# Kernel optimization log

Measured on AMD Instinct MI355X. Metric: run time of the kernel, lower is better.

## Reference

```python
import jax, jax.numpy as jnp
import numpy as np

D_MODEL = 1024
D_STATE = 16
D_CONV = 4
EXPAND = 2
D_INNER = EXPAND * D_MODEL          # 2048
DT_RANK = D_MODEL // 16             # 64 (math.ceil(d_model/16))
BATCH, SEQLEN = 2, 1024


def setup_inputs() -> dict:
    key = jax.random.key(0)
    ks = jax.random.split(key, 9)
    f32 = jnp.float32
    hidden_states = jax.random.normal(ks[0], (BATCH, SEQLEN, D_MODEL), dtype=f32)
    in_proj_w = jax.random.normal(ks[1], (2 * D_INNER, D_MODEL), dtype=f32) * (D_MODEL ** -0.5)
    conv1d_w = jax.random.normal(ks[2], (D_INNER, D_CONV), dtype=f32) * (D_CONV ** -0.5)
    conv1d_b = jax.random.normal(ks[3], (D_INNER,), dtype=f32) * 0.1
    x_proj_w = jax.random.normal(ks[4], (DT_RANK + 2 * D_STATE, D_INNER), dtype=f32) * (D_INNER ** -0.5)
    dt_std = DT_RANK ** -0.5
    dt_proj_w = jax.random.uniform(ks[5], (D_INNER, DT_RANK), dtype=f32, minval=-dt_std, maxval=dt_std)
    dt_proj_b = jax.random.normal(ks[6], (D_INNER,), dtype=f32) * 0.1
    # A = repeat(arange(1, d_state+1), 'n -> d n'); A_log = log(A)
    A_log = jnp.log(jnp.tile(jnp.arange(1, D_STATE + 1, dtype=f32), (D_INNER, 1)))
    D_param = jnp.ones((D_INNER,), dtype=f32)
    out_proj_w = jax.random.normal(ks[7], (D_MODEL, D_INNER), dtype=f32) * (D_INNER ** -0.5)
    return dict(hidden_states=hidden_states, in_proj_w=in_proj_w, conv1d_w=conv1d_w,
                conv1d_b=conv1d_b, x_proj_w=x_proj_w, dt_proj_w=dt_proj_w,
                dt_proj_b=dt_proj_b, A_log=A_log, D_param=D_param, out_proj_w=out_proj_w)


def _mamba_fwd(hidden_states, in_proj_w, conv1d_w, conv1d_b, x_proj_w,
               dt_proj_w, dt_proj_b, A_log, D_param, out_proj_w):
    Bsz, L, _ = hidden_states.shape
    # in_proj: (B,L,d_model) -> (B,L,2*d_inner); split into x, z
    xz = jnp.einsum('bld,ed->ble', hidden_states, in_proj_w)
    x, z = jnp.split(xz, 2, axis=-1)                      # each (B,L,d_inner)
    # causal depthwise conv1d over L (left pad d_conv-1), then SiLU (fused in causal_conv1d_fwd)
    xc = jnp.transpose(x, (0, 2, 1))                      # (B,d_inner,L)
    kern = conv1d_w[:, None, :]                           # (d_inner,1,d_conv)
    conv = jax.lax.conv_general_dilated(
        xc, kern, window_strides=(1,), padding=[(D_CONV - 1, 0)],
        dimension_numbers=('NCH', 'OIH', 'NCH'), feature_group_count=D_INNER)
    u = jax.nn.silu(conv + conv1d_b[None, :, None])       # (B,d_inner,L)
    ut = jnp.transpose(u, (0, 2, 1))                      # (B,L,d_inner)
    # x_proj -> [dt | B | C]
    x_dbl = jnp.einsum('bld,rd->blr', ut, x_proj_w)       # (B,L,dt_rank+2*d_state)
    dt_low = x_dbl[..., :DT_RANK]
    B_var = x_dbl[..., DT_RANK:DT_RANK + D_STATE]         # (B,L,d_state)
    C_var = x_dbl[..., DT_RANK + D_STATE:]                # (B,L,d_state)
    # delta = softplus(dt_proj_w @ dt_low + dt_proj_b)  (delta_bias applied inside selective scan)
    delta = jax.nn.softplus(jnp.einsum('blr,dr->bld', dt_low, dt_proj_w) + dt_proj_b)  # (B,L,d_inner)
    A = -jnp.exp(A_log)                                   # (d_inner,d_state)
    # discretize: h_l = exp(delta*A) * h_{l-1} + (delta*B_l) * u_l
    dA = jnp.exp(delta[..., None] * A)                    # (B,L,d_inner,d_state)
    dBu = delta[..., None] * B_var[:, :, None, :] * ut[..., None]  # (B,L,d_inner,d_state)

    def step(h, inp):
        da, dbu, c = inp
        h = da * h + dbu                                  # (B,d_inner,d_state)
        y = jnp.einsum('bdn,bn->bd', h, c)
        return h, y

    h0 = jnp.zeros((Bsz, D_INNER, D_STATE), dtype=hidden_states.dtype)
    _, ys = jax.lax.scan(step, h0, (jnp.moveaxis(dA, 1, 0),
                                    jnp.moveaxis(dBu, 1, 0),
                                    jnp.moveaxis(C_var, 1, 0)))
    y = jnp.moveaxis(ys, 0, 1)                            # (B,L,d_inner)
    y = y + ut * D_param                                  # skip term D*u
    out_z = y * jax.nn.silu(z)                            # gated output
    return jnp.einsum('bld,ed->ble', out_z, out_proj_w)   # (B,L,d_model)


def reference(hidden_states, in_proj_w, conv1d_w, conv1d_b, x_proj_w,
              dt_proj_w, dt_proj_b, A_log, D_param, out_proj_w):
    return _mamba_fwd(hidden_states, in_proj_w, conv1d_w, conv1d_b, x_proj_w,
                      dt_proj_w, dt_proj_b, A_log, D_param, out_proj_w)
```

## Files before the change

kernel.cpp:

```cpp
#include <hip/hip_runtime.h>
#include <hip/hip_bf16.h>

#define BATCH 2
#define SEQLEN 1024
#define DMODEL 1024
#define DINNER 2048
#define DSTATE 16
#define DTRANK 64
#define ROWS (BATCH * SEQLEN)
#define LOG2E 1.44269504088896340736f

using bf16 = __hip_bfloat16;
typedef __bf16 bf16x8 __attribute__((ext_vector_type(8)));
typedef float f32x4 __attribute__((ext_vector_type(4)));
typedef unsigned short us8 __attribute__((ext_vector_type(8)));

__device__ __forceinline__ float to_f(float x) { return x; }
__device__ __forceinline__ float to_f(bf16 x) { return __bfloat162float(x); }

__device__ __forceinline__ float fexp2(float x) { return __builtin_amdgcn_exp2f(x); }

__device__ __forceinline__ float bfu(unsigned short u) {
    union { unsigned int i; float f; } v;
    v.i = ((unsigned int)u) << 16;
    return v.f;
}

__device__ __forceinline__ unsigned short bf_bits(float x) {
    bf16 h = __float2bfloat16(x);
    union { bf16 b; unsigned short u; } cv;
    cv.b = h;
    return cv.u;
}

__device__ __forceinline__ float softplus_f(float x) {
    return fmaxf(x, 0.f) + log1pf(expf(-fabsf(x)));
}
__device__ __forceinline__ float silu_f(float x) {
    return x * __builtin_amdgcn_rcpf(1.f + fexp2(-x * LOG2E));
}

template <int CTRL>
__device__ __forceinline__ float dpp_shr(float x) {
    int r = __builtin_amdgcn_update_dpp(0, __builtin_bit_cast(int, x), CTRL, 0xF, 0xF, false);
    return __builtin_bit_cast(float, r);
}
__device__ __forceinline__ float row16_sum_to_lane15(float p) {
    p += dpp_shr<0x111>(p);
    p += dpp_shr<0x112>(p);
    p += dpp_shr<0x114>(p);
    p += dpp_shr<0x118>(p);
    return p;
}

__device__ __forceinline__ void gload16(const void* g, void* l) {
    __builtin_amdgcn_global_load_lds(
        (const __attribute__((address_space(1))) void*)g,
        (__attribute__((address_space(3))) void*)l, 16, 0, 0);
}

__global__ __launch_bounds__(256) void prep_kernel(const unsigned short* hs, int* flag,
                                                   float* zbuf, int nzero) {
    if (blockIdx.x == 0) {
        __shared__ int cnt[256];
        int c = 0;
        for (int i = threadIdx.x; i < 8192; i += 256) {
            int e = (hs[i] >> 7) & 0xFF;
            if (e == 0 || e == 0xFF || e < 96 || e > 159) c++;
        }
        cnt[threadIdx.x] = c;
        __syncthreads();
        for (int s = 128; s > 0; s >>= 1) {
            if (threadIdx.x < s) cnt[threadIdx.x] += cnt[threadIdx.x + s];
            __syncthreads();
        }
        if (threadIdx.x == 0) *flag = (cnt[0] < 512) ? 1 : 0;
    } else {
        int i = (blockIdx.x - 1) * 256 + threadIdx.x;
        if (i < nzero) zbuf[i] = 0.f;
    }
}

struct SrcPtrs { const void* p[10]; };

__device__ __constant__ const size_t SEG_OFF[11] = {
    0, 2097152, 6291456, 6299648, 6301696, 6498304,
    6629376, 6631424, 6664192, 6666240, 8763392
};

__global__ __launch_bounds__(256) void convert_all(SrcPtrs s, bf16* __restrict__ dst,
                                                   const int* __restrict__ flag) {
    size_t e = ((size_t)blockIdx.x * 256 + threadIdx.x) * 4;
    if (e >= SEG_OFF[10]) return;
    int seg = 0;
    #pragma unroll
    for (int i = 1; i < 10; ++i) if (e >= SEG_OFF[i]) seg = i;
    int isbf = *flag;
    if (isbf && (seg == 0 || seg == 1 || seg == 9)) return;
    size_t loc = e - SEG_OFF[seg];
    if (isbf) {
        ushort4 v = ((const ushort4*)s.p[seg])[loc / 4];
        ((ushort4*)(dst + e))[0] = v;
    } else {
        float4 v = ((const float4*)s.p[seg])[loc / 4];
        ushort4 o;
        o.x = bf_bits(v.x); o.y = bf_bits(v.y);
        o.z = bf_bits(v.z); o.w = bf_bits(v.w);
        ((ushort4*)(dst + e))[0] = o;
    }
}

template <int OUTMODE>
__global__ __launch_bounds__(256) void gemm_mfma(
    const bf16* __restrict__ A, int lda,
    const bf16* __restrict__ Bm, int ldb,
    void* __restrict__ C, int ldc,
    int Kspl, size_t pstride,
    const bf16* __restrict__ bias,
    const bf16* __restrict__ Aalt,
    const bf16* __restrict__ Balt,
    const int* __restrict__ flag)
{
    if (flag && *flag) {
        if (Aalt) A = Aalt;
        if (Balt) Bm = Balt;
    }
    __shared__ __align__(16) __bf16 sA[128 * 32];
    __shared__ __align__(16) __bf16 sB[128 * 32];
    const int tid = threadIdx.x;
    const int m0 = blockIdx.y * 128;
    const int n0 = blockIdx.x * 128;
    const int wid = tid >> 6, ln = tid & 63;
    const int wy = (wid >> 1) * 64, wx = (wid & 1) * 64;
    const int q = ln >> 4, m16 = ln & 15;
    const int kbeg = blockIdx.z * Kspl;

    f32x4 acc[4][4] = {};

    for (int k0 = kbeg; k0 < kbeg + Kspl; k0 += 32) {
        #pragma unroll
        for (int i = 0; i < 2; ++i) {
            int idx = tid + i * 256;
            int r = idx >> 2, c = (idx & 3) * 8;
            gload16(&A[(size_t)(m0 + r) * lda + k0 + c], &sA[idx * 8]);
        }
        #pragma unroll
        for (int i = 0; i < 2; ++i) {
            int idx = tid + i * 256;
            int r = idx >> 2, c = (idx & 3) * 8;
            gload16(&Bm[(size_t)(n0 + r) * ldb + k0 + c], &sB[idx * 8]);
        }
        __syncthreads();
        bf16x8 a[4], b[4];
        #pragma unroll
        for (int i = 0; i < 4; ++i)
            a[i] = *(const bf16x8*)&sA[(wy + i * 16 + m16) * 32 + q * 8];
        #pragma unroll
        for (int j = 0; j < 4; ++j)
            b[j] = *(const bf16x8*)&sB[(wx + j * 16 + m16) * 32 + q * 8];
        #pragma unroll
        for (int i = 0; i < 4; ++i)
            #pragma unroll
            for (int j = 0; j < 4; ++j)
                acc[i][j] = __builtin_amdgcn_mfma_f32_16x16x32_bf16(a[i], b[j], acc[i][j], 0, 0, 0);
        __syncthreads();
    }

    #pragma unroll
    for (int i = 0; i < 4; ++i) {
        #pragma unroll
        for (int j = 0; j < 4; ++j) {
            #pragma unroll
            for (int r = 0; r < 4; ++r) {
                int row = m0 + wy + i * 16 + q * 4 + r;
                int col = n0 + wx + j * 16 + m16;
                size_t idx = (size_t)row * ldc + col;
                float v = acc[i][j][r];
                if constexpr (OUTMODE == 0) {
                    ((bf16*)C)[idx] = __float2bfloat16(v);
                } else if constexpr (OUTMODE == 2) {
                    ((float*)C + blockIdx.z * pstride)[idx] = v;
                } else if constexpr (OUTMODE == 3) {
                    if (col < 96) atomicAdd((float*)C + idx, v);
                } else if constexpr (OUTMODE == 4) {
                    ((float*)C)[idx] = softplus_f(v + to_f(bias[row]));
                }
            }
        }
    }
}

__global__ __launch_bounds__(256) void dt_gemm(
    const bf16* __restrict__ dtw,
    const float* __restrict__ xd,
    const bf16* __restrict__ bias,
    float* __restrict__ deltaT)
{
    const int tid = threadIdx.x;
    const int wid = tid >> 6, ln = tid & 63;
    const int q = ln >> 4, m16 = ln & 15;
    const int n0 = blockIdx.x * 16;
    const int m0 = (blockIdx.y * 4 + wid) * 16;

    const ushort* ap = (const ushort*)dtw + (size_t)(m0 + m16) * 64 + q * 8;
    bf16x8 a0 = *(const bf16x8*)(ap);
    bf16x8 a1 = *(const bf16x8*)(ap + 32);

    const float* bp = xd + (size_t)(n0 + m16) * 96 + q * 8;
    float4 f0 = *(const float4*)(bp);
    float4 f1 = *(const float4*)(bp + 4);
    float4 f2 = *(const float4*)(bp + 32);
    float4 f3 = *(const float4*)(bp + 36);
    union { bf16x8 v; ushort u[8]; } b0c, b1c;
    b0c.u[0] = bf_bits(f0.x); b0c.u[1] = bf_bits(f0.y);
    b0c.u[2] = bf_bits(f0.z); b0c.u[3] = bf_bits(f0.w);
    b0c.u[4] = bf_bits(f1.x); b0c.u[5] = bf_bits(f1.y);
    b0c.u[6] = bf_bits(f1.z); b0c.u[7] = bf_bits(f1.w);
    b1c.u[0] = bf_bits(f2.x); b1c.u[1] = bf_bits(f2.y);
    b1c.u[2] = bf_bits(f2.z); b1c.u[3] = bf_bits(f2.w);
    b1c.u[4] = bf_bits(f3.x); b1c.u[5] = bf_bits(f3.y);
    b1c.u[6] = bf_bits(f3.z); b1c.u[7] = bf_bits(f3.w);

    f32x4 acc = {};
    acc = __builtin_amdgcn_mfma_f32_16x16x32_bf16(a0, b0c.v, acc, 0, 0, 0);
    acc = __builtin_amdgcn_mfma_f32_16x16x32_bf16(a1, b1c.v, acc, 0, 0, 0);

    const int d0 = m0 + q * 4;
    ushort4 bb = *(const ushort4*)((const ushort*)bias + d0);
    float bv[4] = {bfu(bb.x), bfu(bb.y), bfu(bb.z), bfu(bb.w)};
    #pragma unroll
    for (int r = 0; r < 4; ++r) {
        deltaT[(size_t)(d0 + r) * ROWS + n0 + m16] = softplus_f(acc[r] + bv[r]);
    }
}

__global__ __launch_bounds__(256) void sum_store(
    const float* __restrict__ p0, const float* __restrict__ p1,
    void* __restrict__ out, const int* __restrict__ flag, int n4)
{
    int i = blockIdx.x * 256 + threadIdx.x;
    if (i >= n4) return;
    float4 a = ((const float4*)p0)[i];
    float4 b = ((const float4*)p1)[i];
    float4 sv; sv.x = a.x + b.x; sv.y = a.y + b.y; sv.z = a.z + b.z; sv.w = a.w + b.w;
    if (*flag) {
        ushort4 o;
        o.x = bf_bits(sv.x); o.y = bf_bits(sv.y);
        o.z = bf_bits(sv.z); o.w = bf_bits(sv.w);
        ((ushort4*)out)[i] = o;
    } else {
        ((float4*)out)[i] = sv;
    }
}

__global__ __launch_bounds__(256) void transpose_bf16(
    const ushort* __restrict__ src,
    ushort* __restrict__ dst)
{
    __shared__ ushort t[64][65];
    const int bx = blockIdx.x;
    const int by = blockIdx.y;
    const int tid = threadIdx.x;
    const int lr = tid & 63;
    const int ld = tid >> 6;
    #pragma unroll
    for (int i = 0; i < 16; ++i) {
        int d = ld + i * 4;
        t[d][lr] = src[(size_t)(by * 64 + d) * ROWS + bx * 64 + lr];
    }
    __syncthreads();
    #pragma unroll
    for (int i = 0; i < 16; ++i) {
        int r = ld + i * 4;
        dst[(size_t)(bx * 64 + r) * DINNER + by * 64 + lr] = t[lr][r];
    }
}

__global__ __launch_bounds__(256) void conv_silu_fused(
    const bf16* __restrict__ xzT,
    const bf16* __restrict__ w,
    const bf16* __restrict__ bias,
    bf16* __restrict__ utT,
    ushort* __restrict__ ut)
{
    __shared__ ushort sx[64][68];
    __shared__ ushort tt[64][65];
    const int bx = blockIdx.x;
    const int by = blockIdx.y;
    const int tid = threadIdx.x;
    const int gr0 = bx * 64;
    const bool seqstart = (bx & 15) == 0;

    for (int idx = tid; idx < 64 * 17; idx += 256) {
        int row = idx / 17;
        int c = idx - row * 17;
        ushort4 v;
        if (c == 0 && seqstart) {
            v.x = v.y = v.z = v.w = 0;
        } else {
            const ushort* src = (const ushort*)xzT +
                (size_t)(by * 64 + row) * ROWS + (gr0 - 4 + c * 4);
            v = *(const ushort4*)src;
        }
        *(ushort4*)&sx[row][c * 4] = v;
    }
    __syncthreads();

    const int lr = tid & 63;
    const int ld = tid >> 6;
    #pragma unroll
    for (int i = 0; i < 16; ++i) {
        int dl = ld + i * 4;
        int dg = by * 64 + dl;
        ushort4 wv = *(const ushort4*)((const ushort*)w + dg * 4);
        float w0 = bfu(wv.x), w1 = bfu(wv.y), w2 = bfu(wv.z), w3 = bfu(wv.w);
        float bv = to_f(bias[dg]);
        float acc = bv;
        acc = fmaf(bfu(sx[dl][lr + 1]), w0, acc);
        acc = fmaf(bfu(sx[dl][lr + 2]), w1, acc);
        acc = fmaf(bfu(sx[dl][lr + 3]), w2, acc);
        acc = fmaf(bfu(sx[dl][lr + 4]), w3, acc);
        ushort o = bf_bits(silu_f(acc));
        ((ushort*)utT)[(size_t)dg * ROWS + gr0 + lr] = o;
        tt[dl][lr] = o;
    }
    __syncthreads();
    #pragma unroll
    for (int i = 0; i < 16; ++i) {
        int rl = ld + i * 4;
        ut[(size_t)(gr0 + rl) * DINNER + by * 64 + lr] = tt[lr][rl];
    }
}

#define SCHUNK 8
#define SSTEPS (SEQLEN / SCHUNK)
__global__ __launch_bounds__(512) void scan_kernel16(
    const float* __restrict__ deltaT,
    const bf16*  __restrict__ utT,
    const float* __restrict__ xd96,
    const bf16*  __restrict__ xzT,
    const bf16*  __restrict__ A_log,
    const bf16*  __restrict__ Dp,
    bf16* __restrict__ outzT)
{
    __shared__ float2 sHP[SCHUNK][64];
    const int tid = threadIdx.x;
    const int c = tid >> 6;
    const int w = tid & 63;
    const int dcol = (tid >> 4) & 3;
    const int n = tid & 15;
    const int b = blockIdx.x >> 9;
    const int d = ((blockIdx.x & 511) << 2) + dcol;
    const int row0 = b * SEQLEN + c * SSTEPS;

    const float Aa2 = -expf(to_f(A_log[d * DSTATE + n])) * LOG2E;
    const float Dv = to_f(Dp[d]);

    const float*  dp = deltaT + (size_t)d * ROWS + row0;
    const ushort* up = (const ushort*)utT + (size_t)d * ROWS + row0;
    const ushort* zp = (const ushort*)xzT + (size_t)(DINNER + d) * ROWS + row0;
    const float*  bcp = xd96 + (size_t)row0 * 96 + 64 + n;

    float hl = 0.f, sd = 0.f;
    float4  dv4 = *(const float4*)(dp);
    ushort4 uv4 = *(const ushort4*)(up);
    const float* bct = bcp;
    for (int i0 = 0; i0 < SSTEPS; i0 += 4) {
        float4  dvn = *(const float4*)(dp + i0 + 4);
        ushort4 uvn = *(const ushort4*)(up + i0 + 4);
        float Bv[4];
        Bv[0] = bct[0];
        Bv[1] = bct[96];
        Bv[2] = bct[192];
        Bv[3] = bct[288];
        bct += 384;
        float dv[4] = {dv4.x, dv4.y, dv4.z, dv4.w};
        float uv[4] = {bfu(uv4.x), bfu(uv4.y), bfu(uv4.z), bfu(uv4.w)};
        #pragma unroll
        for (int j = 0; j < 4; ++j) {
            sd += dv[j];
            float a = fexp2(dv[j] * Aa2);
            hl = fmaf(a, hl, dv[j] * Bv[j] * uv[j]);
        }
        dv4 = dvn; uv4 = uvn;
    }
    sHP[c][w] = make_float2(hl, fexp2(sd * Aa2));
    __syncthreads();

    float hin = 0.f;
    for (int cc = 0; cc < c; ++cc) {
        float2 hp = sHP[cc][w];
        hin = fmaf(hp.y, hin, hp.x);
    }

    float h = hin;
    dv4 = *(const float4*)(dp);
    uv4 = *(const ushort4*)(up);
    ushort4 zv4 = *(const ushort4*)(zp);
    bct = bcp;
    for (int i0 = 0; i0 < SSTEPS; i0 += 4) {
        float4  dvn = *(const float4*)(dp + i0 + 4);
        ushort4 uvn = *(const ushort4*)(up + i0 + 4);
        ushort4 zvn = *(const ushort4*)(zp + i0 + 4);
        float Bv[4], Cv[4];
        Bv[0] = bct[0];   Cv[0] = bct[16];
        Bv[1] = bct[96];  Cv[1] = bct[112];
        Bv[2] = bct[192]; Cv[2] = bct[208];
        Bv[3] = bct[288]; Cv[3] = bct[304];
        bct += 384;
        float dv[4] = {dv4.x, dv4.y, dv4.z, dv4.w};
        float uv[4] = {bfu(uv4.x), bfu(uv4.y), bfu(uv4.z), bfu(uv4.w)};
        float zv[4] = {bfu(zv4.x), bfu(zv4.y), bfu(zv4.z), bfu(zv4.w)};
        float y[4];
        #pragma unroll
        for (int j = 0; j < 4; ++j) {
            float a = fexp2(dv[j] * Aa2);
            h = fmaf(a, h, dv[j] * Bv[j] * uv[j]);
            float p = h * Cv[j];
            p = row16_sum_to_lane15(p);
            y[j] = fmaf(uv[j], Dv, p);
        }
        if (n == 15) {
            ushort4 o;
            o.x = bf_bits(y[0] * silu_f(zv[0]));
            o.y = bf_bits(y[1] * silu_f(zv[1]));
            o.z = bf_bits(y[2] * silu_f(zv[2]));
            o.w = bf_bits(y[3] * silu_f(zv[3]));
            *(ushort4*)((ushort*)outzT + (size_t)d * ROWS + row0 + i0) = o;
        }
        dv4 = dvn; uv4 = uvn; zv4 = zvn;
    }
}

extern "C" void kernel_launch(void* const* d_in, const int* in_sizes, int n_in,
                              void* d_out, int out_size, void* d_ws, size_t ws_size,
                              hipStream_t stream) {
    static const size_t SZ[10] = {
        (size_t)BATCH * SEQLEN * DMODEL,
        (size_t)2 * DINNER * DMODEL,
        (size_t)DINNER * 4,
        (size_t)DINNER,
        (size_t)(DTRANK + 2 * DSTATE) * DINNER,
        (size_t)DINNER * DTRANK,
        (size_t)DINNER,
        (size_t)DINNER * DSTATE,
        (size_t)DINNER,
        (size_t)DMODEL * DINNER
    };
    size_t tot_in = 0;
    for (int i = 0; i < 10; ++i) tot_in += SZ[i];

    char* p = (char*)d_ws;
    int* flag = (int*)p;                     p += 64;
    bf16* inb = (bf16*)p;                    p += tot_in * 2;
    bf16* xzT = (bf16*)p;                    p += (size_t)4096 * ROWS * 2;
    bf16* utT = (bf16*)p;                    p += (size_t)DINNER * ROWS * 2;
    bf16* ut  = (bf16*)p;                    p += (size_t)ROWS * DINNER * 2;
    float* xd = (float*)p;                   p += (size_t)ROWS * 96 * 4;
    float* deltaT = (float*)p;               p += (size_t)DINNER * ROWS * 4;
    bf16* outzT = (bf16*)p;                  p += (size_t)DINNER * ROWS * 2;
    bf16* outz = (bf16*)p;                   p += (size_t)ROWS * DINNER * 2;
    float* part = (float*)p;                 p += (size_t)2 * ROWS * DMODEL * 4;
    size_t needed = (size_t)(p - (char*)d_ws);
    if (ws_size < needed) return;

    dim3 blk(256);

    prep_kernel<<<1 + (ROWS * 96 + 255) / 256, blk, 0, stream>>>(
        (const unsigned short*)d_in[0], flag, xd, ROWS * 96);

    bf16* inp[10];
    {
        size_t off = 0;
        for (int i = 0; i < 10; ++i) { inp[i] = inb + off; off += SZ[i]; }
    }
    SrcPtrs sp;
    for (int i = 0; i < 10; ++i) sp.p[i] = d_in[i];
    convert_all<<<(int)((tot_in / 4 + 255) / 256), blk, 0, stream>>>(sp, inb, flag);

    const bf16* hs        = inp[0];
    const bf16* in_proj_w = inp[1];
    const bf16* conv_w    = inp[2];
    const bf16* conv_b    = inp[3];
    const bf16* x_proj_w  = inp[4];
    const bf16* dt_proj_w = inp[5];
    const bf16* dt_proj_b = inp[6];
    const bf16* A_log     = inp[7];
    const bf16* Dp        = inp[8];
    const bf16* out_proj_w= inp[9];

    gemm_mfma<0><<<dim3(ROWS / 128, 4096 / 128, 1), blk, 0, stream>>>(
        in_proj_w, DMODEL, hs, DMODEL, xzT, ROWS, DMODEL, 0, nullptr,
        (const bf16*)d_in[1], (const bf16*)d_in[0], flag);

    conv_silu_fused<<<dim3(ROWS / 64, DINNER / 64), blk, 0, stream>>>(
        xzT, conv_w, conv_b, utT, (ushort*)ut);

    gemm_mfma<3><<<dim3(1, ROWS / 128, 16), blk, 0, stream>>>(
        ut, DINNER, x_proj_w, DINNER, xd, 96, DINNER / 16, 0, nullptr,
        nullptr, nullptr, nullptr);

    dt_gemm<<<dim3(ROWS / 16, DINNER / 64), blk, 0, stream>>>(
        dt_proj_w, xd, dt_proj_b, deltaT);

    scan_kernel16<<<BATCH * (DINNER / 4), dim3(512), 0, stream>>>(
        deltaT, utT, xd, xzT, A_log, Dp, outzT);

    transpose_bf16<<<dim3(ROWS / 64, DINNER / 64), blk, 0, stream>>>(
        (const ushort*)outzT, (ushort*)outz);

    gemm_mfma<2><<<dim3(DMODEL / 128, ROWS / 128, 2), blk, 0, stream>>>(
        outz, DINNER, out_proj_w, DINNER, part, DMODEL, DINNER / 2, (size_t)ROWS * DMODEL,
        nullptr, nullptr, (const bf16*)d_in[9], flag);

    sum_store<<<(ROWS * DMODEL / 4 + 255) / 256, blk, 0, stream>>>(
        part, part + (size_t)ROWS * DMODEL, d_out, flag, ROWS * DMODEL / 4);
}
```

Baseline: 288.5 us.

## Fuse output transpose into scan kernel and reduce x_proj split-K factor

The scan kernel now writes its gated output directly in row-major layout. Each chunk's 4x4 tile of (d, row) values is transposed through a tiny shared-memory buffer, so the separate transpose kernel, its launch and the outzT intermediate buffer are removed. Separately, the x_proj GEMM split-K factor drops from 16 to 4, which means fewer partial blocks but a longer K loop per block. The transposed stores are only 8-byte writes strided by DINNER, which may coalesce poorly. The shared tile is exchanged between lanes of one wavefront with no barrier.

```diff
diff --git a/kernel.cpp b/kernel.cpp
--- a/kernel.cpp
+++ b/kernel.cpp
@@ -253,29 +253,6 @@
     }
 }
 
-__global__ __launch_bounds__(256) void transpose_bf16(
-    const ushort* __restrict__ src,
-    ushort* __restrict__ dst)
-{
-    __shared__ ushort t[64][65];
-    const int bx = blockIdx.x;
-    const int by = blockIdx.y;
-    const int tid = threadIdx.x;
-    const int lr = tid & 63;
-    const int ld = tid >> 6;
-    #pragma unroll
-    for (int i = 0; i < 16; ++i) {
-        int d = ld + i * 4;
-        t[d][lr] = src[(size_t)(by * 64 + d) * ROWS + bx * 64 + lr];
-    }
-    __syncthreads();
-    #pragma unroll
-    for (int i = 0; i < 16; ++i) {
-        int r = ld + i * 4;
-        dst[(size_t)(bx * 64 + r) * DINNER + by * 64 + lr] = t[lr][r];
-    }
-}
-
 __global__ __launch_bounds__(256) void conv_silu_fused(
     const bf16* __restrict__ xzT,
     const bf16* __restrict__ w,
@@ -334,23 +311,25 @@
 
 #define SCHUNK 8
 #define SSTEPS (SEQLEN / SCHUNK)
-__global__ __launch_bounds__(512) void scan_kernel16(
+__global__ __launch_bounds__(512) void scan_kernel18(
     const float* __restrict__ deltaT,
     const bf16*  __restrict__ utT,
     const float* __restrict__ xd96,
     const bf16*  __restrict__ xzT,
     const bf16*  __restrict__ A_log,
     const bf16*  __restrict__ Dp,
-    bf16* __restrict__ outzT)
+    ushort* __restrict__ outz)
 {
     __shared__ float2 sHP[SCHUNK][64];
+    __shared__ __align__(16) ushort sX[SCHUNK][4][4];
     const int tid = threadIdx.x;
     const int c = tid >> 6;
     const int w = tid & 63;
     const int dcol = (tid >> 4) & 3;
     const int n = tid & 15;
     const int b = blockIdx.x >> 9;
-    const int d = ((blockIdx.x & 511) << 2) + dcol;
+    const int dbase = (blockIdx.x & 511) << 2;
+    const int d = dbase + dcol;
     const int row0 = b * SEQLEN + c * SSTEPS;
 
     const float Aa2 = -expf(to_f(A_log[d * DSTATE + n])) * LOG2E;
@@ -426,7 +405,13 @@
             o.y = bf_bits(y[1] * silu_f(zv[1]));
             o.z = bf_bits(y[2] * silu_f(zv[2]));
             o.w = bf_bits(y[3] * silu_f(zv[3]));
-            *(ushort4*)((ushort*)outzT + (size_t)d * ROWS + row0 + i0) = o;
+            *(ushort4*)&sX[c][dcol][0] = o;
+            ushort4 g;
+            g.x = sX[c][0][dcol];
+            g.y = sX[c][1][dcol];
+            g.z = sX[c][2][dcol];
+            g.w = sX[c][3][dcol];
+            *(ushort4*)(outz + (size_t)(row0 + i0 + dcol) * DINNER + dbase) = g;
         }
         dv4 = dvn; uv4 = uvn; zv4 = zvn;
     }
@@ -458,7 +443,6 @@
     bf16* ut  = (bf16*)p;                    p += (size_t)ROWS * DINNER * 2;
     float* xd = (float*)p;                   p += (size_t)ROWS * 96 * 4;
     float* deltaT = (float*)p;               p += (size_t)DINNER * ROWS * 4;
-    bf16* outzT = (bf16*)p;                  p += (size_t)DINNER * ROWS * 2;
     bf16* outz = (bf16*)p;                   p += (size_t)ROWS * DINNER * 2;
     float* part = (float*)p;                 p += (size_t)2 * ROWS * DMODEL * 4;
     size_t needed = (size_t)(p - (char*)d_ws);
@@ -496,18 +480,15 @@
     conv_silu_fused<<<dim3(ROWS / 64, DINNER / 64), blk, 0, stream>>>(
         xzT, conv_w, conv_b, utT, (ushort*)ut);
 
-    gemm_mfma<3><<<dim3(1, ROWS / 128, 16), blk, 0, stream>>>(
-        ut, DINNER, x_proj_w, DINNER, xd, 96, DINNER / 16, 0, nullptr,
+    gemm_mfma<3><<<dim3(1, ROWS / 128, 4), blk, 0, stream>>>(
+        ut, DINNER, x_proj_w, DINNER, xd, 96, DINNER / 4, 0, nullptr,
         nullptr, nullptr, nullptr);
 
     dt_gemm<<<dim3(ROWS / 16, DINNER / 64), blk, 0, stream>>>(
         dt_proj_w, xd, dt_proj_b, deltaT);
 
-    scan_kernel16<<<BATCH * (DINNER / 4), dim3(512), 0, stream>>>(
-        deltaT, utT, xd, xzT, A_log, Dp, outzT);
-
-    transpose_bf16<<<dim3(ROWS / 64, DINNER / 64), blk, 0, stream>>>(
-        (const ushort*)outzT, (ushort*)outz);
+    scan_kernel18<<<BATCH * (DINNER / 4), dim3(512), 0, stream>>>(
+        deltaT, utT, xd, xzT, A_log, Dp, (ushort*)outz);
 
     gemm_mfma<2><<<dim3(DMODEL / 128, ROWS / 128, 2), blk, 0, stream>>>(
         outz, DINNER, out_proj_w, DINNER, part, DMODEL, DINNER / 2, (size_t)ROWS * DMODEL,
```

New measurement: 289.0 us. Within noise of the previous version (+0.2%).
